# Performance work log

Measured on AMD Instinct MI355X. Metric: run time of the kernel, lower is better.

## Reference

```python
import jax, jax.numpy as jnp
import numpy as np

NUM_ANCHORS_LIST = [6400, 1600, 400]  # 640x640 input, strides 8/16/32
TOPK = 9
NUM_CLASSES = 80
EPS = 1e-9


def _make_anchors():
    boxes = []
    for fs, stride in [(80, 8), (40, 16), (20, 32)]:
        c = (np.arange(fs, dtype=np.float32) + 0.5) * stride
        cy, cx = np.meshgrid(c, c, indexing='ij')
        cx = cx.reshape(-1); cy = cy.reshape(-1)
        half = 2.5 * stride  # ATSS-style anchor: 5*stride square
        boxes.append(np.stack([cx - half, cy - half, cx + half, cy + half], axis=-1))
    return jnp.asarray(np.concatenate(boxes, axis=0))  # [8400, 4]


def setup_inputs() -> dict:
    key = jax.random.key(0)
    k1, k2, k3, k4 = jax.random.split(key, 4)
    B, M = 32, 64
    anchor_bboxes = _make_anchors()  # [A,4]
    cxy = jax.random.uniform(k1, (B, M, 2), minval=40.0, maxval=600.0)
    wh = jax.random.uniform(k2, (B, M, 2), minval=10.0, maxval=200.0)
    gt_bboxes = jnp.concatenate([cxy - wh / 2, cxy + wh / 2], axis=-1)  # [B,M,4]
    gt_labels = jax.random.randint(k3, (B, M), 0, NUM_CLASSES)  # int
    pad_gt_mask = jnp.ones((B, M, 1), dtype=jnp.float32)
    pred_bboxes = anchor_bboxes[None] + jax.random.normal(k4, (B, anchor_bboxes.shape[0], 4)) * 4.0
    return {
        'anchor_bboxes': anchor_bboxes,
        'gt_labels': gt_labels,
        'gt_bboxes': gt_bboxes,
        'pad_gt_mask': pad_gt_mask,
        'pred_bboxes': pred_bboxes,
        'bg_index': NUM_CLASSES,
    }


def _bbox_center(b):
    return jnp.stack([(b[..., 0] + b[..., 2]) * 0.5, (b[..., 1] + b[..., 3]) * 0.5], axis=-1)


def _iou(b1, b2):
    # b1 [..., N, 1, 4] vs b2 [..., 1, A, 4] -> [..., N, A]
    x1y1 = jnp.maximum(b1[..., 0:2], b2[..., 0:2])
    x2y2 = jnp.minimum(b1[..., 2:4], b2[..., 2:4])
    overlap = jnp.prod(jnp.maximum(x2y2 - x1y1, 0.0), axis=-1)
    a1 = jnp.prod(jnp.maximum(b1[..., 2:4] - b1[..., 0:2], 0.0), axis=-1)
    a2 = jnp.prod(jnp.maximum(b2[..., 2:4] - b2[..., 0:2], 0.0), axis=-1)
    return overlap / (a1 + a2 - overlap + EPS)


def _check_inside(points, bboxes):
    # points [A,2], bboxes [B,M,4] -> [B,M,A] float mask
    x = points[None, None, :, 0]
    y = points[None, None, :, 1]
    xmin, ymin, xmax, ymax = [bboxes[..., i:i + 1] for i in range(4)]
    ltrb_min = jnp.minimum(jnp.minimum(x - xmin, y - ymin), jnp.minimum(xmax - x, ymax - y))
    return (ltrb_min > EPS).astype(bboxes.dtype)


def _atss_forward(anchor_bboxes, gt_labels, gt_bboxes, pad_gt_mask, pred_bboxes, bg_index):
    B, M, _ = gt_bboxes.shape
    A = anchor_bboxes.shape[0]
    # pairwise IoU [B,M,A]
    ious = _iou(gt_bboxes[:, :, None, :], anchor_bboxes[None, None, :, :])
    gt_centers = _bbox_center(gt_bboxes)          # [B,M,2]
    anchor_centers = _bbox_center(anchor_bboxes)  # [A,2]
    dists = jnp.linalg.norm(gt_centers[:, :, None, :] - anchor_centers[None, None, :, :], axis=-1)  # [B,M,A]

    # per-level topk (smallest distance) + pyramid index offsets
    is_in_topk_list, topk_idx_list = [], []
    start = 0
    for n in NUM_ANCHORS_LIST:
        d = dists[..., start:start + n]
        _, idx = jax.lax.top_k(-d, TOPK)  # [B,M,TOPK], smallest distances
        topk_idx_list.append(idx + start)
        oh = jax.nn.one_hot(idx, n, dtype=dists.dtype).sum(axis=-2) * pad_gt_mask
        is_in_topk_list.append(oh)
        start += n
    is_in_topk = jnp.concatenate(is_in_topk_list, axis=-1)  # [B,M,A]
    topk_idxs = jnp.concatenate(topk_idx_list, axis=-1)     # [B,M,L*TOPK]

    iou_candidates = ious * is_in_topk
    thr = jnp.take_along_axis(iou_candidates, topk_idxs, axis=-1)  # [B,M,27]
    thr_v = thr.mean(axis=-1, keepdims=True) + thr.std(axis=-1, ddof=1, keepdims=True)  # torch.std is unbiased
    is_in_topk = jnp.where(iou_candidates > thr_v, is_in_topk, 0.0)

    is_in_gts = _check_inside(anchor_centers, gt_bboxes)
    mask_positive = is_in_topk * is_in_gts * pad_gt_mask  # [B,M,A]
    mps = mask_positive.sum(axis=-2)                      # [B,A]

    # resolve anchors matched to multiple gts by max IoU (identity when none)
    mask_multi = mps[:, None, :] > 1                       # [B,1,A] broadcast over M
    is_max_iou = jax.nn.one_hot(jnp.argmax(ious, axis=-2), M, dtype=ious.dtype).transpose(0, 2, 1)
    mask_positive = jnp.where(mask_multi, is_max_iou, mask_positive)
    mps = mask_positive.sum(axis=-2)

    assigned_gt_index = jnp.argmax(mask_positive, axis=-2)  # [B,A]
    assigned_labels = jnp.take_along_axis(gt_labels, assigned_gt_index, axis=-1)
    assigned_labels = jnp.where(mps > 0, assigned_labels, bg_index)
    assigned_bboxes = jnp.take_along_axis(gt_bboxes, assigned_gt_index[..., None], axis=1)  # [B,A,4]

    scores = jax.nn.one_hot(assigned_labels, NUM_CLASSES + 1, dtype=jnp.float32)
    keep = jnp.asarray([i for i in range(NUM_CLASSES + 1) if i != bg_index])
    scores = scores[..., keep]  # [B,A,NUM_CLASSES]

    # pred_bboxes branch: modulate scores by max IoU(gt, pred) over positives
    pious = _iou(gt_bboxes[:, :, None, :], pred_bboxes[:, None, :, :]) * mask_positive  # [B,M,A]
    scores = scores * pious.max(axis=-2)[..., None]
    return assigned_labels, assigned_bboxes, scores


def reference(anchor_bboxes, gt_labels, gt_bboxes, pad_gt_mask, pred_bboxes, bg_index):
    return _atss_forward(anchor_bboxes, gt_labels, gt_bboxes, pad_gt_mask, pred_bboxes, bg_index)
```

## Files before the change

### kernel.cpp

```cpp
#include <hip/hip_runtime.h>
#include <cstdint>
#include <cstddef>

#define TOPK 9
#define NCLS 80
#define EPSF 1e-9f

typedef float f4v __attribute__((ext_vector_type(4)));

__device__ __forceinline__ float iou_f(float4 b1, float4 b2) {
    float x1 = fmaxf(b1.x, b2.x), y1 = fmaxf(b1.y, b2.y);
    float x2 = fminf(b1.z, b2.z), y2 = fminf(b1.w, b2.w);
    float ov = fmaxf(x2 - x1, 0.f) * fmaxf(y2 - y1, 0.f);
    float a1 = fmaxf(b1.z - b1.x, 0.f) * fmaxf(b1.w - b1.y, 0.f);
    float a2 = fmaxf(b2.z - b2.x, 0.f) * fmaxf(b2.w - b2.y, 0.f);
    return ov / (a1 + a2 - ov + EPSF);
}

__global__ __launch_bounds__(256) void zero_mask_kernel(unsigned long long* p, int n) {
    int t = blockIdx.x * blockDim.x + threadIdx.x;
    if (t < n) p[t] = 0ull;
}

__global__ __launch_bounds__(192) void atss_topk_kernel(
    const float* __restrict__ anchors,
    const float* __restrict__ gt_bboxes,
    const float* __restrict__ pad_mask,
    unsigned long long* __restrict__ pos_mask,
    int M, int A) {
    const int bm = blockIdx.x;
    const int b = bm / M;
    const int m = bm - b * M;
    const int lane = threadIdx.x & 63;
    const int w = threadIdx.x >> 6;

    const float4 g = ((const float4*)gt_bboxes)[bm];
    const float gcx = (g.x + g.z) * 0.5f;
    const float gcy = (g.y + g.w) * 0.5f;

    __shared__ unsigned idx27[32];
    __shared__ float    iou27[32];

    const int fsL[3]  = {80, 40, 20};
    const int strL[3] = {8, 16, 32};
    const int stL[3]  = {0, 6400, 8000};

    const int fs = fsL[w];
    const float s = (float)strL[w];
    const int st = stL[w];

    int fx = (int)floorf(gcx / s - 0.5f);
    int fy = (int)floorf(gcy / s - 0.5f);
    int ix0 = min(max(fx - 3, 0), fs - 8);
    int iy0 = min(max(fy - 3, 0), fs - 8);

    const int wx = lane & 7;
    const int wy = lane >> 3;
    int gi = st + (iy0 + wy) * fs + (ix0 + wx);
    float4 a = ((const float4*)anchors)[gi];
    float ddx = (a.x + a.z) * 0.5f - gcx;
    float ddy = (a.y + a.w) * 0.5f - gcy;
    float d = sqrtf(ddx * ddx + ddy * ddy);
    unsigned long long key =
        ((unsigned long long)__float_as_uint(d) << 32) | (unsigned)gi;

    int rank = 0;
#pragma unroll
    for (int j = 0; j < 64; ++j) {
        unsigned long long o = __shfl(key, j, 64);
        rank += (o < key) ? 1 : 0;
    }
    if (rank < TOPK)
        idx27[w * TOPK + rank] = (unsigned)(key & 0xFFFFFFFFu);
    __syncthreads();

    if (threadIdx.x < 27) {
        float4 ca = ((const float4*)anchors)[idx27[threadIdx.x]];
        iou27[threadIdx.x] = iou_f(g, ca);
    }
    __syncthreads();

    if (threadIdx.x < 27) {
        float sum = 0.f;
        for (int k = 0; k < 27; ++k) sum += iou27[k];
        float mean = sum * (1.0f / 27.0f);
        float var = 0.f;
        for (int k = 0; k < 27; ++k) {
            float dd = iou27[k] - mean;
            var += dd * dd;
        }
        float thr = mean + sqrtf(var * (1.0f / 26.0f));

        float pad = pad_mask[bm];
        if (pad != 0.f && iou27[threadIdx.x] > thr) {
            unsigned ai = idx27[threadIdx.x];
            float4 ca = ((const float4*)anchors)[ai];
            float acx = (ca.x + ca.z) * 0.5f;
            float acy = (ca.y + ca.w) * 0.5f;
            float lt = fminf(fminf(acx - g.x, acy - g.y),
                             fminf(g.z - acx, g.w - acy));
            if (lt > EPSF) {
                atomicOr(&pos_mask[(size_t)b * A + ai], 1ull << m);
            }
        }
    }
}

__global__ __launch_bounds__(256) void atss_assign_kernel(
    const float* __restrict__ anchors,
    const int*   __restrict__ gt_labels,
    const float* __restrict__ gt_bboxes,
    const float* __restrict__ pred,
    const int*   __restrict__ bg_ptr,
    const unsigned long long* __restrict__ pos_mask,
    float* __restrict__ out_labels,
    float* __restrict__ out_bboxes,
    float* __restrict__ piou_ws,
    int M, int A, int BA) {
    int t = blockIdx.x * blockDim.x + threadIdx.x;
    if (t >= BA) return;
    int b = t / A;
    int a = t - b * A;

    unsigned long long mask = pos_mask[t];
    int mps = __popcll(mask);

    int gt = 0;
    if (mps == 1) {
        gt = __builtin_ctzll(mask);
    } else if (mps > 1) {
        float4 an = ((const float4*)anchors)[a];
        float best = -1.f;
        for (int mm = 0; mm < M; ++mm) {
            float v = iou_f(((const float4*)gt_bboxes)[b * M + mm], an);
            if (v > best) { best = v; gt = mm; }
        }
    }

    float4 gbox = ((const float4*)gt_bboxes)[b * M + gt];
    int label = (mps > 0) ? gt_labels[b * M + gt] : bg_ptr[0];

    out_labels[t] = (float)label;
    ((float4*)out_bboxes)[t] = gbox;

    float pi = 0.f;
    if (mps > 0) {
        float4 p = ((const float4*)pred)[t];
        pi = iou_f(gbox, p);
    }
    piou_ws[t] = pi;
}

__global__ __launch_bounds__(256) void atss_scores_kernel(
    const float* __restrict__ out_labels,
    const float* __restrict__ piou_ws,
    float* __restrict__ scores,
    int total4) {
    int t = blockIdx.x * blockDim.x + threadIdx.x;
    if (t >= total4) return;
    int anchor = t / (NCLS / 4);
    int c0 = (t - anchor * (NCLS / 4)) * 4;
    int label = (int)out_labels[anchor];
    float pi = piou_ws[anchor];
    f4v v;
    v.x = (c0 + 0 == label) ? pi : 0.f;
    v.y = (c0 + 1 == label) ? pi : 0.f;
    v.z = (c0 + 2 == label) ? pi : 0.f;
    v.w = (c0 + 3 == label) ? pi : 0.f;
    __builtin_nontemporal_store(v, (f4v*)scores + t);
}

extern "C" void kernel_launch(void* const* d_in, const int* in_sizes, int n_in,
                              void* d_out, int out_size, void* d_ws, size_t ws_size,
                              hipStream_t stream) {
    const float* anchors   = (const float*)d_in[0];
    const int*   gt_labels = (const int*)d_in[1];
    const float* gt_bboxes = (const float*)d_in[2];
    const float* pad_mask  = (const float*)d_in[3];
    const float* pred      = (const float*)d_in[4];
    const int*   bg_ptr    = (const int*)d_in[5];

    const int A  = in_sizes[0] / 4;
    const int BM = in_sizes[1];
    const int M  = 64;
    const int B  = BM / M;
    const int BA = B * A;

    float* out_labels = (float*)d_out;
    float* out_bboxes = out_labels + (size_t)BA;
    float* scores     = out_bboxes + (size_t)BA * 4;

    unsigned long long* pos_mask = (unsigned long long*)d_ws;
    float* piou_ws = (float*)((char*)d_ws + (size_t)BA * sizeof(unsigned long long));

    zero_mask_kernel<<<(BA + 255) / 256, 256, 0, stream>>>(pos_mask, BA);
    atss_topk_kernel<<<BM, 192, 0, stream>>>(anchors, gt_bboxes, pad_mask,
                                             pos_mask, M, A);
    atss_assign_kernel<<<(BA + 255) / 256, 256, 0, stream>>>(
        anchors, gt_labels, gt_bboxes, pred, bg_ptr, pos_mask,
        out_labels, out_bboxes, piou_ws, M, A, BA);
    const int total4 = BA * (NCLS / 4);
    atss_scores_kernel<<<(total4 + 255) / 256, 256, 0, stream>>>(
        out_labels, piou_ws, scores, total4);
}
```

Measured before the change: 144.5 us.

## Fuse four ATSS kernels into one cooperative kernel with grid syncs

Merges the mask-zeroing, top-k selection, assignment and score-expansion kernels into one persistent cooperative kernel launched with 1024 blocks of 256 threads. Grid-wide syncs replace the kernel boundaries, and each block handles two gt boxes in the top-k phase. This is meant to remove the launch overhead and inter-kernel gaps of four small launches. In exchange it adds grid-sync cost, and the big score-writing phase runs at fixed occupancy.

```diff
diff --git a/kernel.cpp b/kernel.cpp
--- a/kernel.cpp
+++ b/kernel.cpp
@@ -1,6 +1,9 @@
 #include <hip/hip_runtime.h>
+#include <hip/hip_cooperative_groups.h>
 #include <cstdint>
 #include <cstddef>
+
+namespace cg = cooperative_groups;
 
 #define TOPK 9
 #define NCLS 80
@@ -17,157 +20,157 @@
     return ov / (a1 + a2 - ov + EPSF);
 }
 
-__global__ __launch_bounds__(256) void zero_mask_kernel(unsigned long long* p, int n) {
-    int t = blockIdx.x * blockDim.x + threadIdx.x;
-    if (t < n) p[t] = 0ull;
-}
-
-__global__ __launch_bounds__(192) void atss_topk_kernel(
-    const float* __restrict__ anchors,
-    const float* __restrict__ gt_bboxes,
-    const float* __restrict__ pad_mask,
-    unsigned long long* __restrict__ pos_mask,
-    int M, int A) {
-    const int bm = blockIdx.x;
-    const int b = bm / M;
-    const int m = bm - b * M;
-    const int lane = threadIdx.x & 63;
-    const int w = threadIdx.x >> 6;
-
-    const float4 g = ((const float4*)gt_bboxes)[bm];
-    const float gcx = (g.x + g.z) * 0.5f;
-    const float gcy = (g.y + g.w) * 0.5f;
-
-    __shared__ unsigned idx27[32];
-    __shared__ float    iou27[32];
-
-    const int fsL[3]  = {80, 40, 20};
-    const int strL[3] = {8, 16, 32};
-    const int stL[3]  = {0, 6400, 8000};
-
-    const int fs = fsL[w];
-    const float s = (float)strL[w];
-    const int st = stL[w];
-
-    int fx = (int)floorf(gcx / s - 0.5f);
-    int fy = (int)floorf(gcy / s - 0.5f);
-    int ix0 = min(max(fx - 3, 0), fs - 8);
-    int iy0 = min(max(fy - 3, 0), fs - 8);
-
-    const int wx = lane & 7;
-    const int wy = lane >> 3;
-    int gi = st + (iy0 + wy) * fs + (ix0 + wx);
-    float4 a = ((const float4*)anchors)[gi];
-    float ddx = (a.x + a.z) * 0.5f - gcx;
-    float ddy = (a.y + a.w) * 0.5f - gcy;
-    float d = sqrtf(ddx * ddx + ddy * ddy);
-    unsigned long long key =
-        ((unsigned long long)__float_as_uint(d) << 32) | (unsigned)gi;
-
-    int rank = 0;
-#pragma unroll
-    for (int j = 0; j < 64; ++j) {
-        unsigned long long o = __shfl(key, j, 64);
-        rank += (o < key) ? 1 : 0;
-    }
-    if (rank < TOPK)
-        idx27[w * TOPK + rank] = (unsigned)(key & 0xFFFFFFFFu);
-    __syncthreads();
-
-    if (threadIdx.x < 27) {
-        float4 ca = ((const float4*)anchors)[idx27[threadIdx.x]];
-        iou27[threadIdx.x] = iou_f(g, ca);
-    }
-    __syncthreads();
-
-    if (threadIdx.x < 27) {
-        float sum = 0.f;
-        for (int k = 0; k < 27; ++k) sum += iou27[k];
-        float mean = sum * (1.0f / 27.0f);
-        float var = 0.f;
-        for (int k = 0; k < 27; ++k) {
-            float dd = iou27[k] - mean;
-            var += dd * dd;
-        }
-        float thr = mean + sqrtf(var * (1.0f / 26.0f));
-
-        float pad = pad_mask[bm];
-        if (pad != 0.f && iou27[threadIdx.x] > thr) {
-            unsigned ai = idx27[threadIdx.x];
-            float4 ca = ((const float4*)anchors)[ai];
-            float acx = (ca.x + ca.z) * 0.5f;
-            float acy = (ca.y + ca.w) * 0.5f;
-            float lt = fminf(fminf(acx - g.x, acy - g.y),
-                             fminf(g.z - acx, g.w - acy));
-            if (lt > EPSF) {
-                atomicOr(&pos_mask[(size_t)b * A + ai], 1ull << m);
-            }
-        }
-    }
-}
-
-__global__ __launch_bounds__(256) void atss_assign_kernel(
+__global__ __launch_bounds__(256, 4) void atss_fused_kernel(
     const float* __restrict__ anchors,
     const int*   __restrict__ gt_labels,
     const float* __restrict__ gt_bboxes,
+    const float* __restrict__ pad_mask,
     const float* __restrict__ pred,
     const int*   __restrict__ bg_ptr,
-    const unsigned long long* __restrict__ pos_mask,
+    unsigned long long* __restrict__ pos_mask,
+    float* __restrict__ piou_ws,
     float* __restrict__ out_labels,
     float* __restrict__ out_bboxes,
-    float* __restrict__ piou_ws,
-    int M, int A, int BA) {
-    int t = blockIdx.x * blockDim.x + threadIdx.x;
-    if (t >= BA) return;
-    int b = t / A;
-    int a = t - b * A;
-
-    unsigned long long mask = pos_mask[t];
-    int mps = __popcll(mask);
-
-    int gt = 0;
-    if (mps == 1) {
-        gt = __builtin_ctzll(mask);
-    } else if (mps > 1) {
-        float4 an = ((const float4*)anchors)[a];
-        float best = -1.f;
-        for (int mm = 0; mm < M; ++mm) {
-            float v = iou_f(((const float4*)gt_bboxes)[b * M + mm], an);
-            if (v > best) { best = v; gt = mm; }
+    float* __restrict__ scores,
+    int M, int A, int BA, int total4) {
+    cg::grid_group grid = cg::this_grid();
+    const int tid = blockIdx.x * blockDim.x + threadIdx.x;
+    const int nth = gridDim.x * blockDim.x;
+
+    for (int i = tid; i < BA; i += nth) pos_mask[i] = 0ull;
+    grid.sync();
+
+    {
+        __shared__ unsigned idx27[32];
+        __shared__ float    iou27[32];
+        const int lane = threadIdx.x & 63;
+        const int w = threadIdx.x >> 6;
+
+        for (int tt = 0; tt < 2; ++tt) {
+            const int bm = blockIdx.x * 2 + tt;
+            const int b = bm / M;
+            const int m = bm - b * M;
+
+            const float4 g = ((const float4*)gt_bboxes)[bm];
+            const float gcx = (g.x + g.z) * 0.5f;
+            const float gcy = (g.y + g.w) * 0.5f;
+
+            if (w < 3) {
+                const int fsL[3]  = {80, 40, 20};
+                const int strL[3] = {8, 16, 32};
+                const int stL[3]  = {0, 6400, 8000};
+                const int fs = fsL[w];
+                const float s = (float)strL[w];
+                const int st = stL[w];
+
+                int fx = (int)floorf(gcx / s - 0.5f);
+                int fy = (int)floorf(gcy / s - 0.5f);
+                int ix0 = min(max(fx - 3, 0), fs - 8);
+                int iy0 = min(max(fy - 3, 0), fs - 8);
+
+                const int wx = lane & 7;
+                const int wy = lane >> 3;
+                int gi = st + (iy0 + wy) * fs + (ix0 + wx);
+                float4 a = ((const float4*)anchors)[gi];
+                float ddx = (a.x + a.z) * 0.5f - gcx;
+                float ddy = (a.y + a.w) * 0.5f - gcy;
+                float d = sqrtf(ddx * ddx + ddy * ddy);
+                unsigned long long key =
+                    ((unsigned long long)__float_as_uint(d) << 32) |
+                    (unsigned)gi;
+
+                int rank = 0;
+#pragma unroll
+                for (int j = 0; j < 64; ++j) {
+                    unsigned long long o = __shfl(key, j, 64);
+                    rank += (o < key) ? 1 : 0;
+                }
+                if (rank < TOPK)
+                    idx27[w * TOPK + rank] = (unsigned)(key & 0xFFFFFFFFu);
+            }
+            __syncthreads();
+
+            if (threadIdx.x < 27) {
+                float4 ca = ((const float4*)anchors)[idx27[threadIdx.x]];
+                iou27[threadIdx.x] = iou_f(g, ca);
+            }
+            __syncthreads();
+
+            if (threadIdx.x < 27) {
+                float sum = 0.f;
+                for (int k = 0; k < 27; ++k) sum += iou27[k];
+                float mean = sum * (1.0f / 27.0f);
+                float var = 0.f;
+                for (int k = 0; k < 27; ++k) {
+                    float dd = iou27[k] - mean;
+                    var += dd * dd;
+                }
+                float thr = mean + sqrtf(var * (1.0f / 26.0f));
+
+                float pad = pad_mask[bm];
+                if (pad != 0.f && iou27[threadIdx.x] > thr) {
+                    unsigned ai = idx27[threadIdx.x];
+                    float4 ca = ((const float4*)anchors)[ai];
+                    float acx = (ca.x + ca.z) * 0.5f;
+                    float acy = (ca.y + ca.w) * 0.5f;
+                    float lt = fminf(fminf(acx - g.x, acy - g.y),
+                                     fminf(g.z - acx, g.w - acy));
+                    if (lt > EPSF) {
+                        atomicOr(&pos_mask[(size_t)b * A + ai], 1ull << m);
+                    }
+                }
+            }
+            __syncthreads();
         }
     }
-
-    float4 gbox = ((const float4*)gt_bboxes)[b * M + gt];
-    int label = (mps > 0) ? gt_labels[b * M + gt] : bg_ptr[0];
-
-    out_labels[t] = (float)label;
-    ((float4*)out_bboxes)[t] = gbox;
-
-    float pi = 0.f;
-    if (mps > 0) {
-        float4 p = ((const float4*)pred)[t];
-        pi = iou_f(gbox, p);
+    grid.sync();
+
+    for (int t = tid; t < BA; t += nth) {
+        int b = t / A;
+        int a = t - b * A;
+
+        unsigned long long mask = pos_mask[t];
+        int mps = __popcll(mask);
+
+        int gt = 0;
+        if (mps == 1) {
+            gt = __builtin_ctzll(mask);
+        } else if (mps > 1) {
+            float4 an = ((const float4*)anchors)[a];
+            float best = -1.f;
+            for (int mm = 0; mm < M; ++mm) {
+                float v = iou_f(((const float4*)gt_bboxes)[b * M + mm], an);
+                if (v > best) { best = v; gt = mm; }
+            }
+        }
+
+        float4 gbox = ((const float4*)gt_bboxes)[b * M + gt];
+        int label = (mps > 0) ? gt_labels[b * M + gt] : bg_ptr[0];
+
+        out_labels[t] = (float)label;
+        ((float4*)out_bboxes)[t] = gbox;
+
+        float pi = 0.f;
+        if (mps > 0) {
+            float4 p = ((const float4*)pred)[t];
+            pi = iou_f(gbox, p);
+        }
+        piou_ws[t] = pi;
     }
-    piou_ws[t] = pi;
-}
-
-__global__ __launch_bounds__(256) void atss_scores_kernel(
-    const float* __restrict__ out_labels,
-    const float* __restrict__ piou_ws,
-    float* __restrict__ scores,
-    int total4) {
-    int t = blockIdx.x * blockDim.x + threadIdx.x;
-    if (t >= total4) return;
-    int anchor = t / (NCLS / 4);
-    int c0 = (t - anchor * (NCLS / 4)) * 4;
-    int label = (int)out_labels[anchor];
-    float pi = piou_ws[anchor];
-    f4v v;
-    v.x = (c0 + 0 == label) ? pi : 0.f;
-    v.y = (c0 + 1 == label) ? pi : 0.f;
-    v.z = (c0 + 2 == label) ? pi : 0.f;
-    v.w = (c0 + 3 == label) ? pi : 0.f;
-    __builtin_nontemporal_store(v, (f4v*)scores + t);
+    grid.sync();
+
+    for (int t = tid; t < total4; t += nth) {
+        int anchor = t / (NCLS / 4);
+        int c0 = (t - anchor * (NCLS / 4)) * 4;
+        int label = (int)out_labels[anchor];
+        float pi = piou_ws[anchor];
+        f4v v;
+        v.x = (c0 + 0 == label) ? pi : 0.f;
+        v.y = (c0 + 1 == label) ? pi : 0.f;
+        v.z = (c0 + 2 == label) ? pi : 0.f;
+        v.w = (c0 + 3 == label) ? pi : 0.f;
+        __builtin_nontemporal_store(v, (f4v*)scores + t);
+    }
 }
 
 extern "C" void kernel_launch(void* const* d_in, const int* in_sizes, int n_in,
@@ -180,11 +183,12 @@
     const float* pred      = (const float*)d_in[4];
     const int*   bg_ptr    = (const int*)d_in[5];
 
-    const int A  = in_sizes[0] / 4;
-    const int BM = in_sizes[1];
-    const int M  = 64;
-    const int B  = BM / M;
-    const int BA = B * A;
+    int A  = in_sizes[0] / 4;
+    int BM = in_sizes[1];
+    int M  = 64;
+    int B  = BM / M;
+    int BA = B * A;
+    int total4 = BA * (NCLS / 4);
 
     float* out_labels = (float*)d_out;
     float* out_bboxes = out_labels + (size_t)BA;
@@ -193,13 +197,13 @@
     unsigned long long* pos_mask = (unsigned long long*)d_ws;
     float* piou_ws = (float*)((char*)d_ws + (size_t)BA * sizeof(unsigned long long));
 
-    zero_mask_kernel<<<(BA + 255) / 256, 256, 0, stream>>>(pos_mask, BA);
-    atss_topk_kernel<<<BM, 192, 0, stream>>>(anchors, gt_bboxes, pad_mask,
-                                             pos_mask, M, A);
-    atss_assign_kernel<<<(BA + 255) / 256, 256, 0, stream>>>(
-        anchors, gt_labels, gt_bboxes, pred, bg_ptr, pos_mask,
-        out_labels, out_bboxes, piou_ws, M, A, BA);
-    const int total4 = BA * (NCLS / 4);
-    atss_scores_kernel<<<(total4 + 255) / 256, 256, 0, stream>>>(
-        out_labels, piou_ws, scores, total4);
+    void* args[] = {
+        (void*)&anchors, (void*)&gt_labels, (void*)&gt_bboxes,
+        (void*)&pad_mask, (void*)&pred, (void*)&bg_ptr,
+        (void*)&pos_mask, (void*)&piou_ws,
+        (void*)&out_labels, (void*)&out_bboxes, (void*)&scores,
+        (void*)&M, (void*)&A, (void*)&BA, (void*)&total4};
+
+    hipLaunchCooperativeKernel((void*)atss_fused_kernel,
+                               dim3(1024), dim3(256), args, 0, stream);
 }
```

Result: slower. 419.8 us (+190.4%).

## Replace global positive bitmask with per-GT accept lists and fuse assign with scores

Applied to the files above, without the earlier changes.

The top-k kernel now writes a compact list of accepted anchors per GT, counted with a ballot, instead of doing atomicOr into a global B×A bitmask. That removes the zero-fill kernel and the global atomics. The assign and scores kernels are fused into one kernel that tiles anchors in chunks of 525. Each block rebuilds the mask for its chunk in shared memory by scanning all 64 GT lists, then writes labels, boxes and scores directly, skipping the piou and label round-trip through global memory. The cost is that every block rescans all GT lists for its batch, and there are fewer blocks.

```diff
diff --git a/kernel.cpp b/kernel.cpp
--- a/kernel.cpp
+++ b/kernel.cpp
@@ -5,6 +5,7 @@
 #define TOPK 9
 #define NCLS 80
 #define EPSF 1e-9f
+#define CHUNK 525
 
 typedef float f4v __attribute__((ext_vector_type(4)));
 
@@ -17,20 +18,14 @@
     return ov / (a1 + a2 - ov + EPSF);
 }
 
-__global__ __launch_bounds__(256) void zero_mask_kernel(unsigned long long* p, int n) {
-    int t = blockIdx.x * blockDim.x + threadIdx.x;
-    if (t < n) p[t] = 0ull;
-}
-
 __global__ __launch_bounds__(192) void atss_topk_kernel(
     const float* __restrict__ anchors,
     const float* __restrict__ gt_bboxes,
     const float* __restrict__ pad_mask,
-    unsigned long long* __restrict__ pos_mask,
+    int* __restrict__ acc_cnt,
+    int* __restrict__ acc_list,
     int M, int A) {
     const int bm = blockIdx.x;
-    const int b = bm / M;
-    const int m = bm - b * M;
     const int lane = threadIdx.x & 63;
     const int w = threadIdx.x >> 6;
 
@@ -45,33 +40,35 @@
     const int strL[3] = {8, 16, 32};
     const int stL[3]  = {0, 6400, 8000};
 
-    const int fs = fsL[w];
-    const float s = (float)strL[w];
-    const int st = stL[w];
-
-    int fx = (int)floorf(gcx / s - 0.5f);
-    int fy = (int)floorf(gcy / s - 0.5f);
-    int ix0 = min(max(fx - 3, 0), fs - 8);
-    int iy0 = min(max(fy - 3, 0), fs - 8);
-
-    const int wx = lane & 7;
-    const int wy = lane >> 3;
-    int gi = st + (iy0 + wy) * fs + (ix0 + wx);
-    float4 a = ((const float4*)anchors)[gi];
-    float ddx = (a.x + a.z) * 0.5f - gcx;
-    float ddy = (a.y + a.w) * 0.5f - gcy;
-    float d = sqrtf(ddx * ddx + ddy * ddy);
-    unsigned long long key =
-        ((unsigned long long)__float_as_uint(d) << 32) | (unsigned)gi;
-
-    int rank = 0;
+    if (w < 3) {
+        const int fs = fsL[w];
+        const float s = (float)strL[w];
+        const int st = stL[w];
+
+        int fx = (int)floorf(gcx / s - 0.5f);
+        int fy = (int)floorf(gcy / s - 0.5f);
+        int ix0 = min(max(fx - 3, 0), fs - 8);
+        int iy0 = min(max(fy - 3, 0), fs - 8);
+
+        const int wx = lane & 7;
+        const int wy = lane >> 3;
+        int gi = st + (iy0 + wy) * fs + (ix0 + wx);
+        float4 a = ((const float4*)anchors)[gi];
+        float ddx = (a.x + a.z) * 0.5f - gcx;
+        float ddy = (a.y + a.w) * 0.5f - gcy;
+        float d = sqrtf(ddx * ddx + ddy * ddy);
+        unsigned long long key =
+            ((unsigned long long)__float_as_uint(d) << 32) | (unsigned)gi;
+
+        int rank = 0;
 #pragma unroll
-    for (int j = 0; j < 64; ++j) {
-        unsigned long long o = __shfl(key, j, 64);
-        rank += (o < key) ? 1 : 0;
-    }
-    if (rank < TOPK)
-        idx27[w * TOPK + rank] = (unsigned)(key & 0xFFFFFFFFu);
+        for (int j = 0; j < 64; ++j) {
+            unsigned long long o = __shfl(key, j, 64);
+            rank += (o < key) ? 1 : 0;
+        }
+        if (rank < TOPK)
+            idx27[w * TOPK + rank] = (unsigned)(key & 0xFFFFFFFFu);
+    }
     __syncthreads();
 
     if (threadIdx.x < 27) {
@@ -80,6 +77,8 @@
     }
     __syncthreads();
 
+    bool accept = false;
+    unsigned ai = 0;
     if (threadIdx.x < 27) {
         float sum = 0.f;
         for (int k = 0; k < 27; ++k) sum += iou27[k];
@@ -93,81 +92,116 @@
 
         float pad = pad_mask[bm];
         if (pad != 0.f && iou27[threadIdx.x] > thr) {
-            unsigned ai = idx27[threadIdx.x];
+            ai = idx27[threadIdx.x];
             float4 ca = ((const float4*)anchors)[ai];
             float acx = (ca.x + ca.z) * 0.5f;
             float acy = (ca.y + ca.w) * 0.5f;
             float lt = fminf(fminf(acx - g.x, acy - g.y),
                              fminf(g.z - acx, g.w - acy));
-            if (lt > EPSF) {
-                atomicOr(&pos_mask[(size_t)b * A + ai], 1ull << m);
-            }
-        }
-    }
-}
-
-__global__ __launch_bounds__(256) void atss_assign_kernel(
+            accept = (lt > EPSF);
+        }
+    }
+    if (threadIdx.x < 64) {
+        unsigned long long bal = __ballot(accept);
+        if (accept) {
+            int pos = __popcll(bal & ((1ull << threadIdx.x) - 1ull));
+            acc_list[bm * 27 + pos] = (int)ai;
+        }
+        if (threadIdx.x == 0) acc_cnt[bm] = __popcll(bal);
+    }
+}
+
+__global__ __launch_bounds__(256) void atss_assign_scores_kernel(
     const float* __restrict__ anchors,
     const int*   __restrict__ gt_labels,
     const float* __restrict__ gt_bboxes,
     const float* __restrict__ pred,
     const int*   __restrict__ bg_ptr,
-    const unsigned long long* __restrict__ pos_mask,
+    const int*   __restrict__ acc_cnt,
+    const int*   __restrict__ acc_list,
     float* __restrict__ out_labels,
     float* __restrict__ out_bboxes,
-    float* __restrict__ piou_ws,
-    int M, int A, int BA) {
-    int t = blockIdx.x * blockDim.x + threadIdx.x;
-    if (t >= BA) return;
-    int b = t / A;
-    int a = t - b * A;
-
-    unsigned long long mask = pos_mask[t];
-    int mps = __popcll(mask);
-
-    int gt = 0;
-    if (mps == 1) {
-        gt = __builtin_ctzll(mask);
-    } else if (mps > 1) {
-        float4 an = ((const float4*)anchors)[a];
-        float best = -1.f;
-        for (int mm = 0; mm < M; ++mm) {
-            float v = iou_f(((const float4*)gt_bboxes)[b * M + mm], an);
-            if (v > best) { best = v; gt = mm; }
-        }
-    }
-
-    float4 gbox = ((const float4*)gt_bboxes)[b * M + gt];
-    int label = (mps > 0) ? gt_labels[b * M + gt] : bg_ptr[0];
-
-    out_labels[t] = (float)label;
-    ((float4*)out_bboxes)[t] = gbox;
-
-    float pi = 0.f;
-    if (mps > 0) {
-        float4 p = ((const float4*)pred)[t];
-        pi = iou_f(gbox, p);
-    }
-    piou_ws[t] = pi;
-}
-
-__global__ __launch_bounds__(256) void atss_scores_kernel(
-    const float* __restrict__ out_labels,
-    const float* __restrict__ piou_ws,
     float* __restrict__ scores,
-    int total4) {
-    int t = blockIdx.x * blockDim.x + threadIdx.x;
-    if (t >= total4) return;
-    int anchor = t / (NCLS / 4);
-    int c0 = (t - anchor * (NCLS / 4)) * 4;
-    int label = (int)out_labels[anchor];
-    float pi = piou_ws[anchor];
-    f4v v;
-    v.x = (c0 + 0 == label) ? pi : 0.f;
-    v.y = (c0 + 1 == label) ? pi : 0.f;
-    v.z = (c0 + 2 == label) ? pi : 0.f;
-    v.w = (c0 + 3 == label) ? pi : 0.f;
-    __builtin_nontemporal_store(v, (f4v*)scores + t);
+    int M, int A) {
+    __shared__ unsigned mlo[CHUNK];
+    __shared__ unsigned mhi[CHUNK];
+    __shared__ float    slab[CHUNK];
+    __shared__ float    spio[CHUNK];
+
+    const int b = blockIdx.y;
+    const int a0 = blockIdx.x * CHUNK;
+    const int tid = threadIdx.x;
+
+    for (int i = tid; i < CHUNK; i += 256) { mlo[i] = 0u; mhi[i] = 0u; }
+    __syncthreads();
+
+    {
+        const int m = tid >> 2;
+        const int ks = tid & 3;
+        const int bm = b * M + m;
+        const int cnt = acc_cnt[bm];
+        for (int k = ks; k < cnt; k += 4) {
+            int aidx = acc_list[bm * 27 + k];
+            unsigned loc = (unsigned)(aidx - a0);
+            if (loc < (unsigned)CHUNK) {
+                if (m < 32) atomicOr(&mlo[loc], 1u << m);
+                else        atomicOr(&mhi[loc], 1u << (m - 32));
+            }
+        }
+    }
+    __syncthreads();
+
+    const int bg = bg_ptr[0];
+    for (int loc = tid; loc < CHUNK; loc += 256) {
+        const int a = a0 + loc;
+        unsigned long long mask =
+            ((unsigned long long)mhi[loc] << 32) | (unsigned long long)mlo[loc];
+        int mps = __popcll(mask);
+
+        int gt = 0;
+        if (mps == 1) {
+            gt = __builtin_ctzll(mask);
+        } else if (mps > 1) {
+            float4 an = ((const float4*)anchors)[a];
+            float best = -1.f;
+            for (int mm = 0; mm < M; ++mm) {
+                float v = iou_f(((const float4*)gt_bboxes)[b * M + mm], an);
+                if (v > best) { best = v; gt = mm; }
+            }
+        }
+
+        float4 gbox = ((const float4*)gt_bboxes)[b * M + gt];
+        int label = (mps > 0) ? gt_labels[b * M + gt] : bg;
+
+        size_t t = (size_t)b * A + a;
+        __builtin_nontemporal_store((float)label, out_labels + t);
+        f4v gb = {gbox.x, gbox.y, gbox.z, gbox.w};
+        __builtin_nontemporal_store(gb, (f4v*)out_bboxes + t);
+
+        float pi = 0.f;
+        if (mps > 0) {
+            float4 p = ((const float4*)pred)[t];
+            pi = iou_f(gbox, p);
+        }
+        slab[loc] = (float)label;
+        spio[loc] = pi;
+    }
+    __syncthreads();
+
+    const int n4 = CHUNK * (NCLS / 4);
+    const size_t base4 = ((size_t)b * A + a0) * (NCLS / 4);
+    for (int idx = tid; idx < n4; idx += 256) {
+        int loc = idx / (NCLS / 4);
+        int c0 = (idx - loc * (NCLS / 4)) * 4;
+        int label = (int)slab[loc];
+        float pi = spio[loc];
+        f4v v;
+        v.x = (c0 + 0 == label) ? pi : 0.f;
+        v.y = (c0 + 1 == label) ? pi : 0.f;
+        v.z = (c0 + 2 == label) ? pi : 0.f;
+        v.w = (c0 + 3 == label) ? pi : 0.f;
+        __builtin_nontemporal_store(v, (f4v*)scores + base4 + idx);
+    }
 }
 
 extern "C" void kernel_launch(void* const* d_in, const int* in_sizes, int n_in,
@@ -190,16 +224,12 @@
     float* out_bboxes = out_labels + (size_t)BA;
     float* scores     = out_bboxes + (size_t)BA * 4;
 
-    unsigned long long* pos_mask = (unsigned long long*)d_ws;
-    float* piou_ws = (float*)((char*)d_ws + (size_t)BA * sizeof(unsigned long long));
-
-    zero_mask_kernel<<<(BA + 255) / 256, 256, 0, stream>>>(pos_mask, BA);
+    int* acc_cnt  = (int*)d_ws;
+    int* acc_list = acc_cnt + BM;
+
     atss_topk_kernel<<<BM, 192, 0, stream>>>(anchors, gt_bboxes, pad_mask,
-                                             pos_mask, M, A);
-    atss_assign_kernel<<<(BA + 255) / 256, 256, 0, stream>>>(
-        anchors, gt_labels, gt_bboxes, pred, bg_ptr, pos_mask,
-        out_labels, out_bboxes, piou_ws, M, A, BA);
-    const int total4 = BA * (NCLS / 4);
-    atss_scores_kernel<<<(total4 + 255) / 256, 256, 0, stream>>>(
-        out_labels, piou_ws, scores, total4);
-}
+                                             acc_cnt, acc_list, M, A);
+    atss_assign_scores_kernel<<<dim3(A / CHUNK, B), 256, 0, stream>>>(
+        anchors, gt_labels, gt_bboxes, pred, bg_ptr, acc_cnt, acc_list,
+        out_labels, out_bboxes, scores, M, A);
+}
```

Result: faster. 138.2 us (-4.4%).
